# Kernel tuning notes

Hardware: AMD Instinct MI355X
Metric: run time of the kernel (lower is better)

The kernel has to match this reference:

```python
import jax, jax.numpy as jnp
import numpy as np
import math

B, S, D_MODEL, N_HEADS = 4, 2048, 1024, 16
D_HEAD = D_MODEL // N_HEADS

def _xavier(key, shape, gain):
    # nn.init.xavier_uniform_ on [n_heads, fan_in, fan_out]: fan from last two dims
    fan_in, fan_out = shape[-2], shape[-1]
    bound = gain * math.sqrt(6.0 / (fan_in + fan_out))
    return jax.random.uniform(key, shape, jnp.float32, -bound, bound)

def setup_inputs() -> dict:
    key = jax.random.key(0)
    ks = jax.random.split(key, 5)
    g = 1.0 / math.sqrt(2.0)
    return {
        "x": jax.random.normal(ks[0], (B, S, D_MODEL), jnp.float32),
        "W_Q": _xavier(ks[1], (N_HEADS, D_MODEL, D_HEAD), g),
        "W_K": _xavier(ks[2], (N_HEADS, D_MODEL, D_HEAD), g),
        "W_V": _xavier(ks[3], (N_HEADS, D_MODEL, D_HEAD), g),
        "W_O": _xavier(ks[4], (N_HEADS, D_HEAD, D_MODEL), 1.0),
        "b_Q": jnp.zeros((N_HEADS, D_HEAD), jnp.float32),
        "b_K": jnp.zeros((N_HEADS, D_HEAD), jnp.float32),
        "b_V": jnp.zeros((N_HEADS, D_HEAD), jnp.float32),
        "b_O": jnp.zeros((D_MODEL,), jnp.float32),
    }

def reference(x, W_Q, W_K, W_V, W_O, b_Q, b_K, b_V, b_O):
    # q,k,v: [b, s, h, d_head]
    q = jnp.einsum('bsd,hde->bshe', x, W_Q) + b_Q
    k = jnp.einsum('bsd,hde->bshe', x, W_K) + b_K
    v = jnp.einsum('bsd,hde->bshe', x, W_V) + b_V
    scores = jnp.einsum('bqhe,bkhe->bhqk', q, k) / jnp.sqrt(jnp.float32(D_HEAD))
    attn = jax.nn.softmax(scores, axis=-1)  # [b, h, q, k]
    v_out = jnp.einsum('bkhe,bhqk->bqhe', v, attn)
    return jnp.einsum('bqhe,hed->bqd', v_out, W_O) + b_O
```

## Files before the change

kernel.cpp:

```cpp
#include <hip/hip_runtime.h>
#include <hip/hip_bf16.h>
#include <cmath>

#define B_ 4
#define S_ 2048
#define DM_ 1024
#define H_ 16
#define DH_ 64
#define BS_ (B_*S_)

typedef __bf16 bf16x8 __attribute__((ext_vector_type(8)));
typedef __bf16 bf16x4 __attribute__((ext_vector_type(4)));
typedef float  floatx4 __attribute__((ext_vector_type(4)));

__device__ __forceinline__ void gl_lds16(const __bf16* g, __bf16* l) {
  __builtin_amdgcn_global_load_lds(
      (const __attribute__((address_space(1))) void*)g,
      (__attribute__((address_space(3))) void*)l, 16, 0, 0);
}

__global__ void transpose_kernel(const float* __restrict__ src, __bf16* __restrict__ dst,
                                 int R, int C, long srcBatch, long dstBatch) {
  __shared__ __bf16 tile[32][33];
  int b = blockIdx.z;
  long sb = (long)b * srcBatch;
  dst += (long)b * dstBatch;
  int c0 = blockIdx.x * 32, r0 = blockIdx.y * 32;
  int tx = threadIdx.x, ty = threadIdx.y;
  #pragma unroll
  for (int i = 0; i < 32; i += 8)
    tile[ty + i][tx] = (__bf16)src[sb + (long)(r0 + ty + i) * C + (c0 + tx)];
  __syncthreads();
  #pragma unroll
  for (int i = 0; i < 32; i += 8)
    dst[(long)(c0 + ty + i) * R + (r0 + tx)] = tile[tx][ty + i];
}

__global__ void transpose_qkv_kernel(const float* __restrict__ WQ,
                                     const float* __restrict__ WK,
                                     const float* __restrict__ WV,
                                     __bf16* __restrict__ dst) {
  __shared__ __bf16 tile[32][33];
  int z = blockIdx.z;
  int mat = z >> 4, head = z & 15;
  const float* src = (mat == 0 ? WQ : (mat == 1 ? WK : WV)) + (long)head * 65536;
  dst += (long)mat * 1048576 + (long)head * 65536;
  int c0 = blockIdx.x * 32, r0 = blockIdx.y * 32;
  int tx = threadIdx.x, ty = threadIdx.y;
  #pragma unroll
  for (int i = 0; i < 32; i += 8)
    tile[ty + i][tx] = (__bf16)src[(long)(r0 + ty + i) * 64 + (c0 + tx)];
  __syncthreads();
  #pragma unroll
  for (int i = 0; i < 32; i += 8)
    dst[(long)(c0 + ty + i) * 1024 + (r0 + tx)] = tile[tx][ty + i];
}

__global__ void cvt_kernel(const float* __restrict__ src, __bf16* __restrict__ dst) {
  long i = ((long)blockIdx.x * 256 + threadIdx.x) * 8;
  float4 a = *(const float4*)(src + i);
  float4 b = *(const float4*)(src + i + 4);
  bf16x8 t;
  t[0] = (__bf16)a.x; t[1] = (__bf16)a.y; t[2] = (__bf16)a.z; t[3] = (__bf16)a.w;
  t[4] = (__bf16)b.x; t[5] = (__bf16)b.y; t[6] = (__bf16)b.z; t[7] = (__bf16)b.w;
  *(bf16x8*)(dst + i) = t;
}

#define BM 128
#define BN 128
#define BK 64

template<int EPI>
__global__ __launch_bounds__(256, 4) void gemm_kernel(
    const __bf16* __restrict__ A, const __bf16* __restrict__ Bt,
    int M, int N, int K,
    const float* __restrict__ bq, const float* __restrict__ bk,
    const float* __restrict__ bv, const float* __restrict__ bo,
    __bf16* __restrict__ q_ws, __bf16* __restrict__ k_ws,
    __bf16* __restrict__ vT_ws, float* __restrict__ out) {

  __shared__ __align__(16) __bf16 smem[17408];
  __bf16* As = smem;
  __bf16* Bs = smem + 8192;

  int tid  = threadIdx.x;
  int wave = tid >> 6, lane = tid & 63;
  int quad = lane >> 4, l15 = lane & 15;
  int wm = (wave >> 1) * 64, wn = (wave & 1) * 64;

  int nbx = gridDim.x;
  int lid = blockIdx.y * nbx + blockIdx.x;
  int cpx = (nbx * gridDim.y) >> 3;
  int sid = (lid & 7) * cpx + (lid >> 3);
  long m0 = (long)(sid / nbx) * BM;
  long n0 = (long)(sid % nbx) * BN;

  floatx4 acc[4][4] = {};

  int r  = tid >> 3, c8 = tid & 7;
  int cx = c8 ^ (r & 7);
  const __bf16* Asrc = A  + (m0 + r) * (long)K + cx * 8;
  const __bf16* Bsrc = Bt + (n0 + r) * (long)K + cx * 8;

#define STAGE(k0) do {                                                       \
    _Pragma("unroll")                                                        \
    for (int i = 0; i < 4; i++) {                                            \
      gl_lds16(Asrc + (long)(i * 32) * K + (k0), &As[(i * 256 + tid) * 8]);  \
      gl_lds16(Bsrc + (long)(i * 32) * K + (k0), &Bs[(i * 256 + tid) * 8]);  \
    }                                                                        \
  } while (0)

  int swz = l15 & 7;
  const int NT = K / BK;

  STAGE(0);

  for (int t = 0; t < NT; ++t) {
    __syncthreads();

    #pragma unroll
    for (int kk = 0; kk < 2; kk++) {
      bf16x8 af[4], bff[4];
      #pragma unroll
      for (int mt = 0; mt < 4; mt++)
        af[mt] = *(const bf16x8*)(&As[(wm + mt * 16 + l15) * 64 + (((kk * 4 + quad) ^ swz) * 8)]);
      #pragma unroll
      for (int nt = 0; nt < 4; nt++)
        bff[nt] = *(const bf16x8*)(&Bs[(wn + nt * 16 + l15) * 64 + (((kk * 4 + quad) ^ swz) * 8)]);
      #pragma unroll
      for (int mt = 0; mt < 4; mt++)
        #pragma unroll
        for (int nt = 0; nt < 4; nt++)
          acc[mt][nt] = __builtin_amdgcn_mfma_f32_16x16x32_bf16(af[mt], bff[nt], acc[mt][nt], 0, 0, 0);
    }

    if (t + 1 < NT) {
      __syncthreads();
      STAGE((t + 1) * BK);
    }
  }
#undef STAGE

  if (EPI == 0) {
    int seg = (int)(n0 >> 10);
    if (seg < 2) {
      #pragma unroll
      for (int nt = 0; nt < 4; nt++) {
        long n = n0 + wn + nt * 16 + l15;
        int he  = (int)(n & 1023);
        int h = he >> 6, e = he & 63;
        const float* bias = (seg == 0 ? bq : bk);
        float bval = bias[he];
        float scale = (seg == 0 ? 0.125f * 1.44269504088896340f : 1.0f);
        __bf16* dst0 = (seg == 0 ? q_ws : k_ws);
        #pragma unroll
        for (int mt = 0; mt < 4; mt++) {
          #pragma unroll
          for (int rr = 0; rr < 4; rr++) {
            long m = m0 + wm + mt * 16 + quad * 4 + rr;
            int b = (int)(m >> 11), s = (int)(m & 2047);
            float v = (acc[mt][nt][rr] + bval) * scale;
            dst0[((long)(b * 16 + h) * 2048 + s) * 64 + e] = (__bf16)v;
          }
        }
      }
    } else {
      __syncthreads();
      __bf16* vl = smem + wave * 4352;
      #pragma unroll
      for (int nt = 0; nt < 4; nt++) {
        long n = n0 + wn + nt * 16 + l15;
        float bval = bv[(int)(n & 1023)];
        #pragma unroll
        for (int mt = 0; mt < 4; mt++) {
          bf16x4 pw;
          #pragma unroll
          for (int rr = 0; rr < 4; rr++) pw[rr] = (__bf16)(acc[mt][nt][rr] + bval);
          *(bf16x4*)(&vl[(nt * 16 + l15) * 68 + mt * 16 + quad * 4]) = pw;
        }
      }
      asm volatile("s_waitcnt lgkmcnt(0)" ::: "memory");
      int bb = (int)((m0 + wm) >> 11), s0 = (int)((m0 + wm) & 2047);
      #pragma unroll
      for (int rep = 0; rep < 2; rep++) {
        int j = (lane >> 1) + rep * 32;
        long n = n0 + wn + j;
        int he = (int)(n & 1023);
        int h = he >> 6, e = he & 63;
        __bf16* dst = vT_ws + ((long)(bb * 16 + h) * 64 + e) * 2048 + s0 + (lane & 1) * 32;
        const __bf16* srcl = &vl[j * 68 + (lane & 1) * 32];
        #pragma unroll
        for (int c = 0; c < 4; c++)
          *(bf16x8*)(dst + c * 8) = *(const bf16x8*)(srcl + c * 8);
      }
    }
  } else {
    #pragma unroll
    for (int mt = 0; mt < 4; mt++) {
      #pragma unroll
      for (int rr = 0; rr < 4; rr++) {
        long m = m0 + wm + mt * 16 + quad * 4 + rr;
        #pragma unroll
        for (int nt = 0; nt < 4; nt++) {
          long n = n0 + wn + nt * 16 + l15;
          out[m * N + n] = acc[mt][nt][rr] + bo[n];
        }
      }
    }
  }
}

#define KBLK 64

__global__ __launch_bounds__(256, 4) void attn_kernel(
    const __bf16* __restrict__ Q, const __bf16* __restrict__ Kk,
    const __bf16* __restrict__ Vt, __bf16* __restrict__ vout) {

  __shared__ __align__(16) __bf16 Kb[64 * 64];
  __shared__ __align__(16) __bf16 Vb[2][64 * 64];
  __shared__ __align__(16) __bf16 Pb[4][16 * 64];

  int tid = threadIdx.x, wave = tid >> 6, lane = tid & 63;
  int quad = lane >> 4, l15 = lane & 15;

  int id = blockIdx.x;
  int xcd = id & 7, rest = id >> 3;
  int qt = rest & 15, bhhi = rest >> 4;
  int bh = bhhi * 8 + xcd;
  int b = bh >> 4, h = bh & 15;
  int q0 = qt * 128 + wave * 32;

  const __bf16* Qbh = Q  + (long)(b * 16 + h) * 2048 * 64;
  const __bf16* Kbh = Kk + (long)(b * 16 + h) * 2048 * 64;
  const __bf16* Vbh = Vt + (long)(b * 16 + h) * 64 * 2048;

  int rs0 = tid >> 3, cc0 = tid & 7;
  int ccs = cc0 ^ (rs0 & 7);
  const __bf16* Ksrc0 = Kbh + (long)rs0 * 64 + ccs * 8;
  const __bf16* Ksrc1 = Kbh + (long)(rs0 + 32) * 64 + ccs * 8;
  const __bf16* Vsrc0 = Vbh + (long)rs0 * 2048 + ccs * 8;
  const __bf16* Vsrc1 = Vbh + (long)(rs0 + 32) * 2048 + ccs * 8;

#define STAGE_K(kb) do {                                       \
    gl_lds16(Ksrc0 + (long)(kb) * 64, &Kb[tid * 8]);           \
    gl_lds16(Ksrc1 + (long)(kb) * 64, &Kb[tid * 8 + 2048]);    \
  } while (0)
#define STAGE_V(buf, kb) do {                                  \
    gl_lds16(Vsrc0 + (kb), &Vb[buf][tid * 8]);                 \
    gl_lds16(Vsrc1 + (kb), &Vb[buf][tid * 8 + 2048]);          \
  } while (0)

  bf16x8 qf[2][2];
  #pragma unroll
  for (int qh = 0; qh < 2; qh++)
    #pragma unroll
    for (int t = 0; t < 2; t++)
      qf[qh][t] = *(const bf16x8*)(Qbh + (long)(q0 + qh * 16 + l15) * 64 + t * 32 + quad * 8);

  floatx4 o[2][4] = {};
  floatx4 ol[2] = {};
  bf16x8 onesv;
  #pragma unroll
  for (int j = 0; j < 8; j++) onesv[j] = (__bf16)1.0f;

  int swz = l15 & 7;

  STAGE_K(0);
  STAGE_V(0, 0);

  for (int kb = 0; kb < 2048; kb += KBLK) {
    int cur = (kb >> 6) & 1;

    __syncthreads();
    if (kb + KBLK < 2048) STAGE_V(cur ^ 1, kb + KBLK);

    floatx4 sc[2][4];
    __builtin_amdgcn_s_setprio(1);
    #pragma unroll
    for (int nt = 0; nt < 4; nt++) {
      const __bf16* kp = &Kb[(nt * 16 + l15) * 64];
      bf16x8 k0 = *(const bf16x8*)(kp + ((0 + quad) ^ swz) * 8);
      bf16x8 k1 = *(const bf16x8*)(kp + ((4 + quad) ^ swz) * 8);
      #pragma unroll
      for (int qh = 0; qh < 2; qh++) {
        floatx4 z = { 0.f, 0.f, 0.f, 0.f };
        z = __builtin_amdgcn_mfma_f32_16x16x32_bf16(k0, qf[qh][0], z, 0, 0, 0);
        sc[qh][nt] = __builtin_amdgcn_mfma_f32_16x16x32_bf16(k1, qf[qh][1], z, 0, 0, 0);
      }
    }
    __builtin_amdgcn_s_setprio(0);

    asm volatile("s_waitcnt lgkmcnt(0)" ::: "memory");
    __builtin_amdgcn_s_barrier();
    if (kb + KBLK < 2048) STAGE_K(kb + KBLK);

    #pragma unroll
    for (int qh = 0; qh < 2; qh++) {
      #pragma unroll
      for (int nt = 0; nt < 4; nt++) {
        bf16x4 pw;
        #pragma unroll
        for (int rr = 0; rr < 4; rr++)
          pw[rr] = (__bf16)__builtin_amdgcn_exp2f(sc[qh][nt][rr]);
        *(bf16x4*)(&Pb[wave][l15 * 64 + (((nt * 2 + (quad >> 1)) ^ swz) * 8) + (quad & 1) * 4]) = pw;
      }

      __builtin_amdgcn_s_setprio(1);
      #pragma unroll
      for (int t = 0; t < 2; t++) {
        bf16x8 pf = *(const bf16x8*)(&Pb[wave][l15 * 64 + ((t * 4 + quad) ^ swz) * 8]);
        ol[qh] = __builtin_amdgcn_mfma_f32_16x16x32_bf16(onesv, pf, ol[qh], 0, 0, 0);
        #pragma unroll
        for (int dn = 0; dn < 4; dn++) {
          bf16x8 vf = *(const bf16x8*)(&Vb[cur][(dn * 16 + l15) * 64 + ((t * 4 + quad) ^ swz) * 8]);
          o[qh][dn] = __builtin_amdgcn_mfma_f32_16x16x32_bf16(vf, pf, o[qh][dn], 0, 0, 0);
        }
      }
      __builtin_amdgcn_s_setprio(0);
    }
  }
#undef STAGE_K
#undef STAGE_V

  #pragma unroll
  for (int qh = 0; qh < 2; qh++) {
    float rl = 1.f / ol[qh][0];
    int s = q0 + qh * 16 + l15;
    __bf16* outr = vout + ((long)(b * 2048 + s) * 16 + h) * 64;
    #pragma unroll
    for (int dn = 0; dn < 4; dn++) {
      bf16x4 w;
      #pragma unroll
      for (int rr = 0; rr < 4; rr++) w[rr] = (__bf16)(o[qh][dn][rr] * rl);
      *(bf16x4*)(outr + dn * 16 + quad * 4) = w;
    }
  }
}

extern "C" void kernel_launch(void* const* d_in, const int* in_sizes, int n_in,
                              void* d_out, int out_size, void* d_ws, size_t ws_size,
                              hipStream_t stream) {
  const float* x  = (const float*)d_in[0];
  const float* WQ = (const float*)d_in[1];
  const float* WK = (const float*)d_in[2];
  const float* WV = (const float*)d_in[3];
  const float* WO = (const float*)d_in[4];
  const float* bq = (const float*)d_in[5];
  const float* bk = (const float*)d_in[6];
  const float* bv = (const float*)d_in[7];
  const float* bo = (const float*)d_in[8];
  float* out = (float*)d_out;

  uint8_t* ws = (uint8_t*)d_ws;
  const long MB16 = 16777216;
  __bf16* q_ws  = (__bf16*)(ws);
  __bf16* k_ws  = (__bf16*)(ws + 1 * MB16);
  __bf16* vT_ws = (__bf16*)(ws + 2 * MB16);
  __bf16* Wt    = (__bf16*)(ws + 3 * MB16);
  __bf16* vout  = (__bf16*)(ws + 3 * MB16);
  __bf16* WOt   = (__bf16*)(ws);
  __bf16* xb    = (__bf16*)d_out;

  dim3 tb(32, 8);
  transpose_qkv_kernel<<<dim3(2, 32, 48), tb, 0, stream>>>(WQ, WK, WV, Wt);

  cvt_kernel<<<dim3(4096), 256, 0, stream>>>(x, xb);

  gemm_kernel<0><<<dim3(3072 / BN, 8192 / BM), 256, 0, stream>>>(
      xb, Wt, BS_, 3072, DM_, bq, bk, bv, nullptr, q_ws, k_ws, vT_ws, nullptr);

  attn_kernel<<<dim3(1024), 256, 0, stream>>>(q_ws, k_ws, vT_ws, vout);

  transpose_kernel<<<dim3(32, 32, 1), tb, 0, stream>>>(WO, WOt, 1024, 1024, 0, 0);

  gemm_kernel<1><<<dim3(1024 / BN, 8192 / BM), 256, 0, stream>>>(
      vout, WOt, BS_, DM_, DM_, nullptr, nullptr, nullptr, bo, nullptr, nullptr, nullptr, out);
}
```

Before: 270.1 us.

## Add 256x128 double-buffered QKV projection GEMM with 512 threads

Replaces the QKV projection GEMM with a dedicated kernel that computes 256x128 output tiles using 8 waves. It double-buffers the A/B tiles in LDS, prefetching two k-steps ahead with explicit vmcnt waits and barriers, and raises MFMA wave priority with s_setprio. The aim is more reuse of the shared B tile per block and better overlap of global loads with MFMA work. The cost is 96 KB of LDS per block, which limits occupancy to roughly one or two blocks per CU. The old generic GEMM is trimmed to serve only the output projection.

```diff
diff --git a/kernel.cpp b/kernel.cpp
--- a/kernel.cpp
+++ b/kernel.cpp
@@ -66,6 +66,146 @@
   *(bf16x8*)(dst + i) = t;
 }
 
+__global__ __launch_bounds__(512, 2) void gemm256_kernel(
+    const __bf16* __restrict__ A, const __bf16* __restrict__ Bt,
+    const float* __restrict__ bq, const float* __restrict__ bk,
+    const float* __restrict__ bv,
+    __bf16* __restrict__ q_ws, __bf16* __restrict__ k_ws,
+    __bf16* __restrict__ vT_ws) {
+  const int K = 1024;
+  __shared__ __align__(16) __bf16 smem[49152];
+  __bf16* As = smem;
+  __bf16* Bs = smem + 32768;
+
+  int tid = threadIdx.x;
+  int wave = tid >> 6, lane = tid & 63;
+  int quad = lane >> 4, l15 = lane & 15;
+  int wr = wave >> 1, wc = wave & 1;
+  int wm = wr * 64, wn = wc * 64;
+
+  int nbx = gridDim.x;
+  int lid = blockIdx.y * nbx + blockIdx.x;
+  int cpx = (nbx * gridDim.y) >> 3;
+  int sid = (lid & 7) * cpx + (lid >> 3);
+  long m0 = (long)(sid / nbx) * 256;
+  long n0 = (long)(sid % nbx) * 128;
+
+  floatx4 acc[4][4] = {};
+
+  int r = tid >> 3, c8 = tid & 7;
+  int cx = c8 ^ (r & 7);
+  const __bf16* Asrc = A  + (m0 + r) * (long)K + cx * 8;
+  const __bf16* Bsrc = Bt + (n0 + r) * (long)K + cx * 8;
+
+#define STAGE256(s, k0) do {                                                  \
+    _Pragma("unroll")                                                         \
+    for (int i = 0; i < 4; i++)                                               \
+      gl_lds16(Asrc + (long)(i * 64) * K + (k0),                              \
+               &As[(s) * 16384 + (i * 512 + tid) * 8]);                       \
+    _Pragma("unroll")                                                         \
+    for (int i = 0; i < 2; i++)                                               \
+      gl_lds16(Bsrc + (long)(i * 64) * K + (k0),                              \
+               &Bs[(s) * 8192 + (i * 512 + tid) * 8]);                        \
+  } while (0)
+
+  int swz = l15 & 7;
+  const int NT = 16;
+
+  STAGE256(0, 0);
+  STAGE256(1, 64);
+  asm volatile("s_waitcnt vmcnt(6)" ::: "memory");
+  __builtin_amdgcn_s_barrier();
+  __builtin_amdgcn_sched_barrier(0);
+
+  for (int t = 0; t < NT; ++t) {
+    int s = t & 1;
+    const __bf16* Ab = &As[s * 16384];
+    const __bf16* Bb = &Bs[s * 8192];
+    #pragma unroll
+    for (int kk = 0; kk < 2; kk++) {
+      bf16x8 af[4], bf[4];
+      #pragma unroll
+      for (int mt = 0; mt < 4; mt++)
+        af[mt] = *(const bf16x8*)(&Ab[(wm + mt * 16 + l15) * 64 + (((kk * 4 + quad) ^ swz) * 8)]);
+      #pragma unroll
+      for (int nt = 0; nt < 4; nt++)
+        bf[nt] = *(const bf16x8*)(&Bb[(wn + nt * 16 + l15) * 64 + (((kk * 4 + quad) ^ swz) * 8)]);
+      __builtin_amdgcn_s_setprio(1);
+      #pragma unroll
+      for (int mt = 0; mt < 4; mt++)
+        #pragma unroll
+        for (int nt = 0; nt < 4; nt++)
+          acc[mt][nt] = __builtin_amdgcn_mfma_f32_16x16x32_bf16(af[mt], bf[nt], acc[mt][nt], 0, 0, 0);
+      __builtin_amdgcn_s_setprio(0);
+    }
+    asm volatile("s_waitcnt lgkmcnt(0)" ::: "memory");
+    __builtin_amdgcn_s_barrier();
+    __builtin_amdgcn_sched_barrier(0);
+    if (t + 2 < NT) {
+      STAGE256(s, (t + 2) * 64);
+      asm volatile("s_waitcnt vmcnt(6)" ::: "memory");
+    } else {
+      asm volatile("s_waitcnt vmcnt(0)" ::: "memory");
+    }
+    __builtin_amdgcn_s_barrier();
+    __builtin_amdgcn_sched_barrier(0);
+  }
+#undef STAGE256
+
+  int seg = (int)(n0 >> 10);
+  if (seg < 2) {
+    #pragma unroll
+    for (int nt = 0; nt < 4; nt++) {
+      long n = n0 + wn + nt * 16 + l15;
+      int he = (int)(n & 1023);
+      int h = he >> 6, e = he & 63;
+      const float* bias = (seg == 0 ? bq : bk);
+      float bval = bias[he];
+      float scale = (seg == 0 ? 0.125f * 1.44269504088896340f : 1.0f);
+      __bf16* dst0 = (seg == 0 ? q_ws : k_ws);
+      #pragma unroll
+      for (int mt = 0; mt < 4; mt++) {
+        #pragma unroll
+        for (int rr = 0; rr < 4; rr++) {
+          long m = m0 + wm + mt * 16 + quad * 4 + rr;
+          int b = (int)(m >> 11), sI = (int)(m & 2047);
+          float v = (acc[mt][nt][rr] + bval) * scale;
+          dst0[((long)(b * 16 + h) * 2048 + sI) * 64 + e] = (__bf16)v;
+        }
+      }
+    }
+  } else {
+    __syncthreads();
+    __bf16* vl = smem + wave * 4352;
+    #pragma unroll
+    for (int nt = 0; nt < 4; nt++) {
+      long n = n0 + wn + nt * 16 + l15;
+      float bval = bv[(int)(n & 1023)];
+      #pragma unroll
+      for (int mt = 0; mt < 4; mt++) {
+        bf16x4 pw;
+        #pragma unroll
+        for (int rr = 0; rr < 4; rr++) pw[rr] = (__bf16)(acc[mt][nt][rr] + bval);
+        *(bf16x4*)(&vl[(nt * 16 + l15) * 68 + mt * 16 + quad * 4]) = pw;
+      }
+    }
+    asm volatile("s_waitcnt lgkmcnt(0)" ::: "memory");
+    int bb = (int)((m0 + wm) >> 11), s0 = (int)((m0 + wm) & 2047);
+    #pragma unroll
+    for (int rep = 0; rep < 2; rep++) {
+      int j = (lane >> 1) + rep * 32;
+      long n = n0 + wn + j;
+      int he = (int)(n & 1023);
+      int h = he >> 6, e = he & 63;
+      __bf16* dst = vT_ws + ((long)(bb * 16 + h) * 64 + e) * 2048 + s0 + (lane & 1) * 32;
+      const __bf16* srcl = &vl[j * 68 + (lane & 1) * 32];
+      #pragma unroll
+      for (int c = 0; c < 4; c++)
+        *(bf16x8*)(dst + c * 8) = *(const bf16x8*)(srcl + c * 8);
+    }
+  }
+}
+
 #define BM 128
 #define BN 128
 #define BK 64
@@ -74,12 +214,9 @@
 __global__ __launch_bounds__(256, 4) void gemm_kernel(
     const __bf16* __restrict__ A, const __bf16* __restrict__ Bt,
     int M, int N, int K,
-    const float* __restrict__ bq, const float* __restrict__ bk,
-    const float* __restrict__ bv, const float* __restrict__ bo,
-    __bf16* __restrict__ q_ws, __bf16* __restrict__ k_ws,
-    __bf16* __restrict__ vT_ws, float* __restrict__ out) {
-
-  __shared__ __align__(16) __bf16 smem[17408];
+    const float* __restrict__ bo, float* __restrict__ out) {
+
+  __shared__ __align__(16) __bf16 smem[16384];
   __bf16* As = smem;
   __bf16* Bs = smem + 8192;
 
@@ -141,70 +278,15 @@
   }
 #undef STAGE
 
-  if (EPI == 0) {
-    int seg = (int)(n0 >> 10);
-    if (seg < 2) {
+  #pragma unroll
+  for (int mt = 0; mt < 4; mt++) {
+    #pragma unroll
+    for (int rr = 0; rr < 4; rr++) {
+      long m = m0 + wm + mt * 16 + quad * 4 + rr;
       #pragma unroll
       for (int nt = 0; nt < 4; nt++) {
         long n = n0 + wn + nt * 16 + l15;
-        int he  = (int)(n & 1023);
-        int h = he >> 6, e = he & 63;
-        const float* bias = (seg == 0 ? bq : bk);
-        float bval = bias[he];
-        float scale = (seg == 0 ? 0.125f * 1.44269504088896340f : 1.0f);
-        __bf16* dst0 = (seg == 0 ? q_ws : k_ws);
-        #pragma unroll
-        for (int mt = 0; mt < 4; mt++) {
-          #pragma unroll
-          for (int rr = 0; rr < 4; rr++) {
-            long m = m0 + wm + mt * 16 + quad * 4 + rr;
-            int b = (int)(m >> 11), s = (int)(m & 2047);
-            float v = (acc[mt][nt][rr] + bval) * scale;
-            dst0[((long)(b * 16 + h) * 2048 + s) * 64 + e] = (__bf16)v;
-          }
-        }
-      }
-    } else {
-      __syncthreads();
-      __bf16* vl = smem + wave * 4352;
-      #pragma unroll
-      for (int nt = 0; nt < 4; nt++) {
-        long n = n0 + wn + nt * 16 + l15;
-        float bval = bv[(int)(n & 1023)];
-        #pragma unroll
-        for (int mt = 0; mt < 4; mt++) {
-          bf16x4 pw;
-          #pragma unroll
-          for (int rr = 0; rr < 4; rr++) pw[rr] = (__bf16)(acc[mt][nt][rr] + bval);
-          *(bf16x4*)(&vl[(nt * 16 + l15) * 68 + mt * 16 + quad * 4]) = pw;
-        }
-      }
-      asm volatile("s_waitcnt lgkmcnt(0)" ::: "memory");
-      int bb = (int)((m0 + wm) >> 11), s0 = (int)((m0 + wm) & 2047);
-      #pragma unroll
-      for (int rep = 0; rep < 2; rep++) {
-        int j = (lane >> 1) + rep * 32;
-        long n = n0 + wn + j;
-        int he = (int)(n & 1023);
-        int h = he >> 6, e = he & 63;
-        __bf16* dst = vT_ws + ((long)(bb * 16 + h) * 64 + e) * 2048 + s0 + (lane & 1) * 32;
-        const __bf16* srcl = &vl[j * 68 + (lane & 1) * 32];
-        #pragma unroll
-        for (int c = 0; c < 4; c++)
-          *(bf16x8*)(dst + c * 8) = *(const bf16x8*)(srcl + c * 8);
-      }
-    }
-  } else {
-    #pragma unroll
-    for (int mt = 0; mt < 4; mt++) {
-      #pragma unroll
-      for (int rr = 0; rr < 4; rr++) {
-        long m = m0 + wm + mt * 16 + quad * 4 + rr;
-        #pragma unroll
-        for (int nt = 0; nt < 4; nt++) {
-          long n = n0 + wn + nt * 16 + l15;
-          out[m * N + n] = acc[mt][nt][rr] + bo[n];
-        }
+        out[m * N + n] = acc[mt][nt][rr] + bo[n];
       }
     }
   }
@@ -366,13 +448,13 @@
 
   cvt_kernel<<<dim3(4096), 256, 0, stream>>>(x, xb);
 
-  gemm_kernel<0><<<dim3(3072 / BN, 8192 / BM), 256, 0, stream>>>(
-      xb, Wt, BS_, 3072, DM_, bq, bk, bv, nullptr, q_ws, k_ws, vT_ws, nullptr);
+  gemm256_kernel<<<dim3(3072 / 128, 8192 / 256), 512, 0, stream>>>(
+      xb, Wt, bq, bk, bv, q_ws, k_ws, vT_ws);
 
   attn_kernel<<<dim3(1024), 256, 0, stream>>>(q_ws, k_ws, vT_ws, vout);
 
   transpose_kernel<<<dim3(32, 32, 1), tb, 0, stream>>>(WO, WOt, 1024, 1024, 0, 0);
 
   gemm_kernel<1><<<dim3(1024 / BN, 8192 / BM), 256, 0, stream>>>(
-      vout, WOt, BS_, DM_, DM_, nullptr, nullptr, nullptr, bo, nullptr, nullptr, nullptr, out);
-}
+      vout, WOt, BS_, DM_, DM_, bo, out);
+}
```

New measurement: 276.5 us. 1.02x slower.
